# Optimization experiments

Measured on AMD Instinct MI355X. Metric: run time of the kernel, lower is better.

Reference implementation:

```python
import jax, jax.numpy as jnp
import numpy as np

NUM_CLASS = 31
B = 4096
F_IN = 2048
F_BOT = 256


def setup_inputs() -> dict:
    key = jax.random.key(0)
    ks = jax.random.split(key, 6)
    return {
        "source": jax.random.normal(ks[0], (B, F_IN), dtype=jnp.float32),
        "target": jax.random.normal(ks[1], (B, F_IN), dtype=jnp.float32),
        "W_b": jax.random.normal(ks[2], (F_IN, F_BOT), dtype=jnp.float32) * (1.0 / np.sqrt(F_IN)),
        "b_b": jnp.zeros((F_BOT,), dtype=jnp.float32),
        "W_c": jax.random.normal(ks[3], (F_BOT, NUM_CLASS), dtype=jnp.float32) * (1.0 / np.sqrt(F_BOT)),
        "b_c": jnp.zeros((NUM_CLASS,), dtype=jnp.float32),
        "source_label": jax.random.randint(ks[4], (B,), 0, NUM_CLASS, dtype=jnp.int64),
    }


def _conf_margin(logits, labels):
    # get_confidence_output_margin: softmax confidence margin vs best wrong class
    conf = jax.nn.softmax(logits, axis=-1)
    mask = jax.nn.one_hot(labels, NUM_CLASS, dtype=conf.dtype)
    targets_conf = jnp.sum(conf * mask, axis=1)
    max_excl_conf = jnp.max(conf * (1.0 - mask), axis=1)
    return targets_conf - max_excl_conf


def _pairwise_sqdist(s, t):
    # ||x_p - x_q||^2 computed as a single GEMM + broadcast (replaces python double loop)
    s2 = jnp.sum(s * s, axis=1)  # [Bs]
    t2 = jnp.sum(t * t, axis=1)  # [Bt]
    d2 = s2[:, None] + t2[None, :] - 2.0 * (s @ t.T)
    return jnp.maximum(d2, 0.0)


def reference(source, target, W_b, b_b, W_c, b_c, source_label):
    # bottleneck: Linear + ReLU (shared weights for both domains)
    src = jax.nn.relu(source @ W_b + b_b)  # [B, 256]
    tar = jax.nn.relu(target @ W_b + b_b)  # [B, 256]

    src_clf = src @ W_c + b_c  # [B, 31]
    tar_clf = tar @ W_c + b_c  # [B, 31]

    # cross entropy on source
    logp = jax.nn.log_softmax(src_clf, axis=-1)
    clf_loss = -jnp.mean(jnp.take_along_axis(logp, source_label[:, None], axis=1))

    src_margin = _conf_margin(src_clf, source_label)
    tar_margin = _conf_margin(tar_clf, jnp.argmax(tar_clf, axis=1))

    # no_grad diagnostics: MMD + Gaussian kernel means (amplitude=1, sigma in {1,5})
    delta = jnp.mean(src, axis=0) - jnp.mean(tar, axis=0)
    curr_mmd = jax.lax.stop_gradient(delta @ delta)
    d2 = _pairwise_sqdist(src, tar)  # [B, B]
    curr_gk1 = jax.lax.stop_gradient(jnp.mean(jnp.exp(-0.5 * d2)))
    curr_gk5 = jax.lax.stop_gradient(jnp.mean(jnp.exp(-d2 / 50.0)))

    return jnp.concatenate([
        jnp.stack([clf_loss, curr_mmd, curr_gk1, curr_gk5]),
        src_margin,
        tar_margin,
    ])  # [4 + 2B]
```

## Files before the change

kernel.cpp:

```cpp
#include <hip/hip_runtime.h>
#include <stdint.h>

#define DI __device__ __forceinline__

typedef float f32x4 __attribute__((ext_vector_type(4)));
typedef short bf16x8 __attribute__((ext_vector_type(8)));

DI uint16_t f2bf(float f) {
    union { float f; uint32_t u; } v; v.f = f;
    uint32_t r = v.u + 0x7FFF + ((v.u >> 16) & 1);
    return (uint16_t)(r >> 16);
}
DI float bf2f(uint16_t h) {
    union { uint32_t u; float f; } v; v.u = ((uint32_t)h) << 16;
    return v.f;
}
DI void gl_lds16(const void* g, void* l) {
    __builtin_amdgcn_global_load_lds(
        (__attribute__((address_space(1))) void*)(uintptr_t)g,
        (__attribute__((address_space(3))) void*)(uintptr_t)l,
        16, 0, 0);
}

__global__ void k_init(const float* __restrict__ Wc, uint16_t* __restrict__ WcT,
                       float* __restrict__ accs) {
    int tid = threadIdx.x;
    if (tid < 4) accs[tid] = 0.f;
    for (int idx = tid; idx < 32 * 256; idx += 256) {
        int n = idx >> 8, k = idx & 255;
        WcT[idx] = (n < 31) ? f2bf(Wc[k * 31 + n]) : (uint16_t)0;
    }
}

__global__ void k_transpose_wb(const float* __restrict__ Wb, uint16_t* __restrict__ WbT) {
    __shared__ float t[32][33];
    int kb = blockIdx.x, nb = blockIdx.y;
    int tx = threadIdx.x & 31, ty0 = (threadIdx.x >> 5) * 4;
    for (int i = 0; i < 4; ++i)
        t[ty0 + i][tx] = Wb[(kb * 32 + ty0 + i) * 256 + nb * 32 + tx];
    __syncthreads();
    for (int i = 0; i < 4; ++i)
        WbT[(nb * 32 + ty0 + i) * 2048 + kb * 32 + tx] = f2bf(t[tx][ty0 + i]);
}

__launch_bounds__(256)
__global__ void k_bottleneck(const float* __restrict__ src, const float* __restrict__ tgt,
                             const uint16_t* __restrict__ WbT, const float* __restrict__ bb,
                             uint16_t* __restrict__ Y) {
    __shared__ __align__(16) uint8_t lds[40960];
    int tid = threadIdx.x;
    int lane = tid & 63, w = tid >> 6;
    int bm = blockIdx.x >> 1, bn = blockIdx.x & 1;
    int m0 = bm * 32;
    const float* X = (m0 < 4096) ? (src + (size_t)m0 * 2048)
                                 : (tgt + (size_t)(m0 - 4096) * 2048);
    int ar = tid >> 3, akb = (tid >> 2) & 1, ap = tid & 3;
    int ac = ap ^ (ar & 3) ^ ((ar >> 2) & 3);
    const float* Ag = X + ar * 2048 + akb * 32 + ac * 8;
    const int AwOff = akb * 2048 + ar * 64 + ap * 16;
    int cc = (lane >> 4) ^ (lane & 3) ^ ((lane >> 2) & 3);
    const uint16_t* Bg0; const uint16_t* Bg1; const uint16_t* Bg2; const uint16_t* Bg3;
    {
        int p = lane & 3;
        int i0 = w * 4;
        #define BGADDR(ii) ({ int s_ = i0 + (ii); int kb_ = s_ >> 3; \
            int r_ = (s_ & 7) * 16 + (lane >> 2); \
            int c_ = p ^ (r_ & 3) ^ ((r_ >> 2) & 3); \
            WbT + (size_t)(bn * 128 + r_) * 2048 + kb_ * 32 + c_ * 8; })
        Bg0 = BGADDR(0); Bg1 = BGADDR(1); Bg2 = BGADDR(2); Bg3 = BGADDR(3);
        #undef BGADDR
    }
    const int lbB = 8192 + w * 4096;

    f32x4 acc[2][2] = {};
    float4 rE0, rE1, rO0, rO1;

    #define STAGE_B(par, k0) do { \
        gl_lds16(Bg0 + (k0), lds + lbB + (par) * 16384 + 0);    \
        gl_lds16(Bg1 + (k0), lds + lbB + (par) * 16384 + 1024); \
        gl_lds16(Bg2 + (k0), lds + lbB + (par) * 16384 + 2048); \
        gl_lds16(Bg3 + (k0), lds + lbB + (par) * 16384 + 3072); \
    } while (0)

    #define WRITE_A(par, r0v, r1v) do { \
        uint4 u_; \
        u_.x = (uint32_t)f2bf((r0v).x) | ((uint32_t)f2bf((r0v).y) << 16); \
        u_.y = (uint32_t)f2bf((r0v).z) | ((uint32_t)f2bf((r0v).w) << 16); \
        u_.z = (uint32_t)f2bf((r1v).x) | ((uint32_t)f2bf((r1v).y) << 16); \
        u_.w = (uint32_t)f2bf((r1v).z) | ((uint32_t)f2bf((r1v).w) << 16); \
        *(uint4*)(lds + (par) * 4096 + AwOff) = u_; \
    } while (0)

    #define COMPUTE(par) do { \
        _Pragma("unroll") \
        for (int kb = 0; kb < 2; ++kb) { \
            bf16x8 a_[2], b_[2]; \
            _Pragma("unroll") \
            for (int mi = 0; mi < 2; ++mi) \
                a_[mi] = *(const bf16x8*)(lds + (par) * 4096 + kb * 2048 + \
                                          (mi * 16 + (lane & 15)) * 64 + cc * 16); \
            _Pragma("unroll") \
            for (int nf = 0; nf < 2; ++nf) \
                b_[nf] = *(const bf16x8*)(lds + 8192 + (par) * 16384 + kb * 8192 + \
                                          (w * 32 + nf * 16 + (lane & 15)) * 64 + cc * 16); \
            _Pragma("unroll") \
            for (int mi = 0; mi < 2; ++mi) \
                _Pragma("unroll") \
                for (int nf = 0; nf < 2; ++nf) \
                    acc[mi][nf] = __builtin_amdgcn_mfma_f32_16x16x32_bf16( \
                        a_[mi], b_[nf], acc[mi][nf], 0, 0, 0); \
        } \
    } while (0)

    #define FENCE() asm volatile("" ::: "memory")

    STAGE_B(0, 0);
    FENCE();
    rE0 = *(const float4*)(Ag);
    rE1 = *(const float4*)(Ag + 4);
    FENCE();
    rO0 = *(const float4*)(Ag + 64);
    rO1 = *(const float4*)(Ag + 68);
    asm volatile("s_waitcnt vmcnt(2)" ::: "memory");
    WRITE_A(0, rE0, rE1);
    asm volatile("s_waitcnt lgkmcnt(0)" ::: "memory");
    __builtin_amdgcn_s_barrier();

    for (int tt = 0; tt < 15; ++tt) {
        {
            int t = 2 * tt;
            STAGE_B(1, (t + 1) * 64);
            FENCE();
            rE0 = *(const float4*)(Ag + (t + 2) * 64);
            rE1 = *(const float4*)(Ag + (t + 2) * 64 + 4);
            FENCE();
            COMPUTE(0);
            asm volatile("s_waitcnt vmcnt(6)" ::: "memory");
            WRITE_A(1, rO0, rO1);
            asm volatile("s_waitcnt vmcnt(2) lgkmcnt(0)" ::: "memory");
            __builtin_amdgcn_s_barrier();
        }
        {
            int t = 2 * tt + 1;
            STAGE_B(0, (t + 1) * 64);
            FENCE();
            rO0 = *(const float4*)(Ag + (t + 2) * 64);
            rO1 = *(const float4*)(Ag + (t + 2) * 64 + 4);
            FENCE();
            COMPUTE(1);
            asm volatile("s_waitcnt vmcnt(6)" ::: "memory");
            WRITE_A(0, rE0, rE1);
            asm volatile("s_waitcnt vmcnt(2) lgkmcnt(0)" ::: "memory");
            __builtin_amdgcn_s_barrier();
        }
    }
    STAGE_B(1, 31 * 64);
    FENCE();
    COMPUTE(0);
    asm volatile("s_waitcnt vmcnt(4)" ::: "memory");
    WRITE_A(1, rO0, rO1);
    asm volatile("s_waitcnt vmcnt(0) lgkmcnt(0)" ::: "memory");
    __builtin_amdgcn_s_barrier();
    COMPUTE(1);

    #undef STAGE_B
    #undef WRITE_A
    #undef COMPUTE
    #undef FENCE

    for (int mi = 0; mi < 2; ++mi)
        for (int nf = 0; nf < 2; ++nf) {
            int col = bn * 128 + w * 32 + nf * 16 + (lane & 15);
            float bias = bb[col];
            for (int j = 0; j < 4; ++j) {
                int row = m0 + mi * 16 + (lane >> 4) * 4 + j;
                float v = acc[mi][nf][j] + bias;
                v = fmaxf(v, 0.f);
                Y[(size_t)row * 256 + col] = f2bf(v);
            }
        }
}

__launch_bounds__(256)
__global__ void k_stats(const uint16_t* __restrict__ Y, float* __restrict__ s2t2,
                        float* __restrict__ colsum_part) {
    __shared__ float cs[4][256];
    int tid = threadIdx.x, lane = tid & 63, w = tid >> 6;
    int r0 = blockIdx.x * 32 + w * 8;
    float c0 = 0.f, c1 = 0.f, c2 = 0.f, c3 = 0.f;
    for (int i = 0; i < 8; ++i) {
        int row = r0 + i;
        ushort4 v = *(const ushort4*)(Y + (size_t)row * 256 + lane * 4);
        float a = bf2f(v.x), b = bf2f(v.y), c = bf2f(v.z), d = bf2f(v.w);
        c0 += a; c1 += b; c2 += c; c3 += d;
        float s = a * a + b * b + c * c + d * d;
        for (int m = 1; m < 64; m <<= 1) s += __shfl_xor(s, m);
        if (lane == 0) s2t2[row] = s;
    }
    cs[w][lane * 4 + 0] = c0;
    cs[w][lane * 4 + 1] = c1;
    cs[w][lane * 4 + 2] = c2;
    cs[w][lane * 4 + 3] = c3;
    __syncthreads();
    colsum_part[blockIdx.x * 256 + tid] =
        cs[0][tid] + cs[1][tid] + cs[2][tid] + cs[3][tid];
}

__launch_bounds__(256)
__global__ void k_classifier(const uint16_t* __restrict__ Y, const uint16_t* __restrict__ WcT,
                             const float* __restrict__ bc, const int* __restrict__ labels,
                             float* __restrict__ out_margin, float* __restrict__ ce_acc) {
    __shared__ __align__(16) uint8_t lds[49152];
    int tid = threadIdx.x, lane = tid & 63, w = tid >> 6;
    int m0 = blockIdx.x * 64;
    int cc = (lane >> 4) ^ (lane & 3) ^ ((lane >> 2) & 3);
    for (int s = w; s < 48; s += 4) {
        int r, p, c;
        if (s < 32) {
            int kb = s >> 2, r0 = (s & 3) * 16;
            r = r0 + (lane >> 2); p = lane & 3;
            c = p ^ (r & 3) ^ ((r >> 2) & 3);
            gl_lds16(Y + (size_t)(m0 + r) * 256 + kb * 32 + c * 8, lds + s * 1024);
        } else {
            int s2 = s - 32;
            int kb = s2 >> 1, r0 = (s2 & 1) * 16;
            r = r0 + (lane >> 2); p = lane & 3;
            c = p ^ (r & 3) ^ ((r >> 2) & 3);
            gl_lds16(WcT + r * 256 + kb * 32 + c * 8, lds + 32768 + s2 * 1024);
        }
    }
    __syncthreads();
    f32x4 acc[2] = {};
    for (int kb = 0; kb < 8; ++kb) {
        int r = w * 16 + (lane & 15);
        bf16x8 a = *(const bf16x8*)(lds + kb * 4096 + r * 64 + cc * 16);
        for (int nf = 0; nf < 2; ++nf) {
            int rn = nf * 16 + (lane & 15);
            bf16x8 b = *(const bf16x8*)(lds + 32768 + kb * 2048 + rn * 64 + cc * 16);
            acc[nf] = __builtin_amdgcn_mfma_f32_16x16x32_bf16(a, b, acc[nf], 0, 0, 0);
        }
    }
    int c0 = lane & 15, c1 = 16 + c0;
    float bc0 = bc[c0];
    float bc1 = (c1 < 31) ? bc[c1] : 0.f;
    bool is_src = (m0 < 4096);
    float ce_local = 0.f;
    for (int j = 0; j < 4; ++j) {
        int row = m0 + w * 16 + (lane >> 4) * 4 + j;
        float v0 = acc[0][j] + bc0;
        float v1 = (c1 < 31) ? (acc[1][j] + bc1) : -1e30f;
        float mx = fmaxf(v0, v1);
        for (int m = 1; m < 16; m <<= 1) mx = fmaxf(mx, __shfl_xor(mx, m, 16));
        float e0 = __expf(v0 - mx);
        float e1 = (c1 < 31) ? __expf(v1 - mx) : 0.f;
        float ssum = e0 + e1;
        for (int m = 1; m < 16; m <<= 1) ssum += __shfl_xor(ssum, m, 16);
        float inv = 1.f / ssum;
        float conf0 = e0 * inv, conf1 = e1 * inv;
        int lab;
        if (is_src) {
            lab = labels[row];
        } else {
            float bv; int bi;
            if (v0 >= v1) { bv = v0; bi = c0; } else { bv = v1; bi = c1; }
            for (int m = 1; m < 16; m <<= 1) {
                float ov = __shfl_xor(bv, m, 16);
                int oi = __shfl_xor(bi, m, 16);
                if (ov > bv || (ov == bv && oi < bi)) { bv = ov; bi = oi; }
            }
            lab = bi;
        }
        float tc = (c0 == lab ? conf0 : 0.f) + (c1 == lab ? conf1 : 0.f);
        for (int m = 1; m < 16; m <<= 1) tc += __shfl_xor(tc, m, 16);
        float ex = fmaxf(c0 == lab ? -1.f : conf0,
                         (c1 == lab || c1 >= 31) ? -1.f : conf1);
        for (int m = 1; m < 16; m <<= 1) ex = fmaxf(ex, __shfl_xor(ex, m, 16));
        if (c0 == 0) out_margin[row] = tc - ex;
        if (is_src) {
            float vl = (c0 == lab) ? v0 : ((c1 == lab) ? v1 : -1e30f);
            for (int m = 1; m < 16; m <<= 1) vl = fmaxf(vl, __shfl_xor(vl, m, 16));
            if (c0 == 0) ce_local += -(vl - mx - __logf(ssum));
        }
    }
    if (is_src) {
        ce_local += __shfl_xor(ce_local, 16);
        ce_local += __shfl_xor(ce_local, 32);
        if (lane == 0) atomicAdd(ce_acc, ce_local);
    }
}

__launch_bounds__(256)
__global__ void k_pairwise(const uint16_t* __restrict__ Y, const float* __restrict__ s2t2,
                           float* __restrict__ gk_part) {
    __shared__ __align__(16) uint8_t lds[65536];
    int tid = threadIdx.x, lane = tid & 63, w = tid >> 6;
    int m0 = blockIdx.x * 128, n0 = blockIdx.y * 128;
    int cc = (lane >> 4) ^ (lane & 3) ^ ((lane >> 2) & 3);
    int wm = (w & 1) * 64, wn = (w >> 1) * 64;
    f32x4 acc[4][4] = {};
    for (int h = 0; h < 2; ++h) {
        if (h) __syncthreads();
        int k0 = h * 128;
        for (int i = 0; i < 8; ++i) {
            int s = w * 8 + i;
            int kb = s >> 3, r0 = (s & 7) * 16;
            int r = r0 + (lane >> 2), p = lane & 3;
            int c = p ^ (r & 3) ^ ((r >> 2) & 3);
            gl_lds16(Y + (size_t)(m0 + r) * 256 + k0 + kb * 32 + c * 8, lds + s * 1024);
            gl_lds16(Y + (size_t)(4096 + n0 + r) * 256 + k0 + kb * 32 + c * 8,
                     lds + 32768 + s * 1024);
        }
        __syncthreads();
        for (int kb = 0; kb < 4; ++kb) {
            bf16x8 a[4], b[4];
            for (int mi = 0; mi < 4; ++mi) {
                int r = wm + mi * 16 + (lane & 15);
                a[mi] = *(const bf16x8*)(lds + kb * 8192 + r * 64 + cc * 16);
            }
            for (int nf = 0; nf < 4; ++nf) {
                int rn = wn + nf * 16 + (lane & 15);
                b[nf] = *(const bf16x8*)(lds + 32768 + kb * 8192 + rn * 64 + cc * 16);
            }
            for (int mi = 0; mi < 4; ++mi)
                for (int nf = 0; nf < 4; ++nf)
                    acc[mi][nf] = __builtin_amdgcn_mfma_f32_16x16x32_bf16(
                        a[mi], b[nf], acc[mi][nf], 0, 0, 0);
        }
    }
    float t2v[4];
    for (int nf = 0; nf < 4; ++nf)
        t2v[nf] = s2t2[4096 + n0 + wn + nf * 16 + (lane & 15)];
    float g1 = 0.f, g5 = 0.f;
    for (int mi = 0; mi < 4; ++mi) {
        int rbase = m0 + wm + mi * 16 + (lane >> 4) * 4;
        float s2v[4];
        for (int j = 0; j < 4; ++j) s2v[j] = s2t2[rbase + j];
        for (int nf = 0; nf < 4; ++nf)
            for (int j = 0; j < 4; ++j) {
                float d2 = s2v[j] + t2v[nf] - 2.f * acc[mi][nf][j];
                d2 = fmaxf(d2, 0.f);
                g1 += __expf(-0.5f * d2);
                g5 += __expf(-0.02f * d2);
            }
    }
    for (int m = 1; m < 64; m <<= 1) { g1 += __shfl_xor(g1, m); g5 += __shfl_xor(g5, m); }
    __syncthreads();
    float* red = (float*)lds;
    if (lane == 0) { red[w * 2] = g1; red[w * 2 + 1] = g5; }
    __syncthreads();
    if (tid == 0) {
        int bid = blockIdx.y * 32 + blockIdx.x;
        gk_part[bid * 2]     = red[0] + red[2] + red[4] + red[6];
        gk_part[bid * 2 + 1] = red[1] + red[3] + red[5] + red[7];
    }
}

__global__ void k_finalize(const float* __restrict__ colsum_part,
                           const float* __restrict__ gk_part,
                           const float* __restrict__ accs, float* __restrict__ d_out) {
    __shared__ float red[12];
    int tid = threadIdx.x, lane = tid & 63, w = tid >> 6;
    float cs = 0.f, ct = 0.f;
    for (int b = 0; b < 128; ++b)   cs += colsum_part[b * 256 + tid];
    for (int b = 128; b < 256; ++b) ct += colsum_part[b * 256 + tid];
    float delta = (cs - ct) * (1.f / 4096.f);
    float sq = delta * delta;
    float g1 = 0.f, g5 = 0.f;
    for (int i = 0; i < 4; ++i) {
        int p = tid * 4 + i;
        g1 += gk_part[p * 2];
        g5 += gk_part[p * 2 + 1];
    }
    for (int m = 1; m < 64; m <<= 1) {
        sq += __shfl_xor(sq, m);
        g1 += __shfl_xor(g1, m);
        g5 += __shfl_xor(g5, m);
    }
    if (lane == 0) { red[w * 3] = sq; red[w * 3 + 1] = g1; red[w * 3 + 2] = g5; }
    __syncthreads();
    if (tid == 0) {
        d_out[0] = accs[0] * (1.f / 4096.f);
        d_out[1] = red[0] + red[3] + red[6] + red[9];
        d_out[2] = (red[1] + red[4] + red[7] + red[10]) * 5.9604644775390625e-08f;
        d_out[3] = (red[2] + red[5] + red[8] + red[11]) * 5.9604644775390625e-08f;
    }
}

extern "C" void kernel_launch(void* const* d_in, const int* in_sizes, int n_in,
                              void* d_out, int out_size, void* d_ws, size_t ws_size,
                              hipStream_t stream) {
    const float* source = (const float*)d_in[0];
    const float* target = (const float*)d_in[1];
    const float* Wb     = (const float*)d_in[2];
    const float* bb     = (const float*)d_in[3];
    const float* Wc     = (const float*)d_in[4];
    const float* bc     = (const float*)d_in[5];
    const int*   labels = (const int*)d_in[6];
    float* out = (float*)d_out;
    uint8_t* ws = (uint8_t*)d_ws;

    uint16_t* Y    = (uint16_t*)(ws);
    uint16_t* WbT  = (uint16_t*)(ws + 4194304);
    uint16_t* WcT  = (uint16_t*)(ws + 5242880);
    float*    s2t2 = (float*)(ws + 5259264);
    float*    accs = (float*)(ws + 5292032);
    float*    colsum_part = (float*)(ws + 4194304);
    float*    gk_part     = (float*)(ws + 4194304 + 262144);

    k_init<<<1, 256, 0, stream>>>(Wc, WcT, accs);
    k_transpose_wb<<<dim3(64, 8), 256, 0, stream>>>(Wb, WbT);
    k_bottleneck<<<512, 256, 0, stream>>>(source, target, WbT, bb, Y);
    k_stats<<<256, 256, 0, stream>>>(Y, s2t2, colsum_part);
    k_classifier<<<128, 256, 0, stream>>>(Y, WcT, bc, labels, out + 4, accs);
    k_pairwise<<<dim3(32, 32), 256, 0, stream>>>(Y, s2t2, gk_part);
    k_finalize<<<1, 256, 0, stream>>>(colsum_part, gk_part, accs, out);
}
```

Before: 174.6 us.

## Narrow bottleneck GEMM N-tile to 64 and triple-buffer W_b staging

The bottleneck GEMM tile shrinks from 32x128 to 32x64 per block, which doubles the grid to 1024 blocks and cuts LDS per block to 32 KB so more blocks fit on each CU. The B operand staging moves from double to triple buffering with a two-stage-ahead prefetch and uniform vmcnt(4) waits, unrolled by six to rotate buffers. The cost is that each A row block (the fp32 activations) is now loaded and converted four times instead of twice, which raises global traffic on the dominant 64 MB input read.

```diff
diff --git a/kernel.cpp b/kernel.cpp
--- a/kernel.cpp
+++ b/kernel.cpp
@@ -47,10 +47,10 @@
 __global__ void k_bottleneck(const float* __restrict__ src, const float* __restrict__ tgt,
                              const uint16_t* __restrict__ WbT, const float* __restrict__ bb,
                              uint16_t* __restrict__ Y) {
-    __shared__ __align__(16) uint8_t lds[40960];
+    __shared__ __align__(16) uint8_t lds[32768];
     int tid = threadIdx.x;
     int lane = tid & 63, w = tid >> 6;
-    int bm = blockIdx.x >> 1, bn = blockIdx.x & 1;
+    int bm = blockIdx.x >> 2, bn = blockIdx.x & 3;
     int m0 = bm * 32;
     const float* X = (m0 < 4096) ? (src + (size_t)m0 * 2048)
                                  : (tgt + (size_t)(m0 - 4096) * 2048);
@@ -59,27 +59,27 @@
     const float* Ag = X + ar * 2048 + akb * 32 + ac * 8;
     const int AwOff = akb * 2048 + ar * 64 + ap * 16;
     int cc = (lane >> 4) ^ (lane & 3) ^ ((lane >> 2) & 3);
-    const uint16_t* Bg0; const uint16_t* Bg1; const uint16_t* Bg2; const uint16_t* Bg3;
+    const uint16_t* Bg0; const uint16_t* Bg1;
+    int lb0, lb1;
     {
         int p = lane & 3;
-        int i0 = w * 4;
-        #define BGADDR(ii) ({ int s_ = i0 + (ii); int kb_ = s_ >> 3; \
-            int r_ = (s_ & 7) * 16 + (lane >> 2); \
+        #define BGADDR(ii) ({ int s_ = w * 2 + (ii); int kb_ = s_ >> 2; \
+            int r_ = (s_ & 3) * 16 + (lane >> 2); \
             int c_ = p ^ (r_ & 3) ^ ((r_ >> 2) & 3); \
-            WbT + (size_t)(bn * 128 + r_) * 2048 + kb_ * 32 + c_ * 8; })
-        Bg0 = BGADDR(0); Bg1 = BGADDR(1); Bg2 = BGADDR(2); Bg3 = BGADDR(3);
+            WbT + (size_t)(bn * 64 + r_) * 2048 + kb_ * 32 + c_ * 8; })
+        Bg0 = BGADDR(0); Bg1 = BGADDR(1);
         #undef BGADDR
-    }
-    const int lbB = 8192 + w * 4096;
-
-    f32x4 acc[2][2] = {};
+        lb0 = (w * 2 + 0) * 1024;
+        lb1 = (w * 2 + 1) * 1024;
+    }
+    int rnOff = (w * 16 + (lane & 15)) * 64 + cc * 16;
+
+    f32x4 acc[2] = {};
     float4 rE0, rE1, rO0, rO1;
 
-    #define STAGE_B(par, k0) do { \
-        gl_lds16(Bg0 + (k0), lds + lbB + (par) * 16384 + 0);    \
-        gl_lds16(Bg1 + (k0), lds + lbB + (par) * 16384 + 1024); \
-        gl_lds16(Bg2 + (k0), lds + lbB + (par) * 16384 + 2048); \
-        gl_lds16(Bg3 + (k0), lds + lbB + (par) * 16384 + 3072); \
+    #define STAGE_B(buf, k0) do { \
+        gl_lds16(Bg0 + (k0), lds + 8192 + (buf) * 8192 + lb0); \
+        gl_lds16(Bg1 + (k0), lds + 8192 + (buf) * 8192 + lb1); \
     } while (0)
 
     #define WRITE_A(par, r0v, r1v) do { \
@@ -91,94 +91,89 @@
         *(uint4*)(lds + (par) * 4096 + AwOff) = u_; \
     } while (0)
 
-    #define COMPUTE(par) do { \
+    #define COMPUTE(buf, par) do { \
         _Pragma("unroll") \
         for (int kb = 0; kb < 2; ++kb) { \
-            bf16x8 a_[2], b_[2]; \
+            bf16x8 a_[2], b_; \
             _Pragma("unroll") \
             for (int mi = 0; mi < 2; ++mi) \
                 a_[mi] = *(const bf16x8*)(lds + (par) * 4096 + kb * 2048 + \
                                           (mi * 16 + (lane & 15)) * 64 + cc * 16); \
-            _Pragma("unroll") \
-            for (int nf = 0; nf < 2; ++nf) \
-                b_[nf] = *(const bf16x8*)(lds + 8192 + (par) * 16384 + kb * 8192 + \
-                                          (w * 32 + nf * 16 + (lane & 15)) * 64 + cc * 16); \
+            b_ = *(const bf16x8*)(lds + 8192 + (buf) * 8192 + kb * 4096 + rnOff); \
             _Pragma("unroll") \
             for (int mi = 0; mi < 2; ++mi) \
-                _Pragma("unroll") \
-                for (int nf = 0; nf < 2; ++nf) \
-                    acc[mi][nf] = __builtin_amdgcn_mfma_f32_16x16x32_bf16( \
-                        a_[mi], b_[nf], acc[mi][nf], 0, 0, 0); \
+                acc[mi] = __builtin_amdgcn_mfma_f32_16x16x32_bf16( \
+                    a_[mi], b_, acc[mi], 0, 0, 0); \
         } \
     } while (0)
 
     #define FENCE() asm volatile("" ::: "memory")
+    #define WAIT4() asm volatile("s_waitcnt vmcnt(4)" ::: "memory")
+    #define WAIT0() asm volatile("s_waitcnt vmcnt(0)" ::: "memory")
+    #define LGKM0_BAR() do { asm volatile("s_waitcnt lgkmcnt(0)" ::: "memory"); \
+                             __builtin_amdgcn_s_barrier(); } while (0)
 
     STAGE_B(0, 0);
     FENCE();
     rE0 = *(const float4*)(Ag);
     rE1 = *(const float4*)(Ag + 4);
     FENCE();
+    STAGE_B(1, 64);
+    FENCE();
     rO0 = *(const float4*)(Ag + 64);
     rO1 = *(const float4*)(Ag + 68);
-    asm volatile("s_waitcnt vmcnt(2)" ::: "memory");
+    WAIT4();
     WRITE_A(0, rE0, rE1);
-    asm volatile("s_waitcnt lgkmcnt(0)" ::: "memory");
-    __builtin_amdgcn_s_barrier();
-
-    for (int tt = 0; tt < 15; ++tt) {
-        {
-            int t = 2 * tt;
-            STAGE_B(1, (t + 1) * 64);
-            FENCE();
-            rE0 = *(const float4*)(Ag + (t + 2) * 64);
-            rE1 = *(const float4*)(Ag + (t + 2) * 64 + 4);
-            FENCE();
-            COMPUTE(0);
-            asm volatile("s_waitcnt vmcnt(6)" ::: "memory");
-            WRITE_A(1, rO0, rO1);
-            asm volatile("s_waitcnt vmcnt(2) lgkmcnt(0)" ::: "memory");
-            __builtin_amdgcn_s_barrier();
-        }
-        {
-            int t = 2 * tt + 1;
-            STAGE_B(0, (t + 1) * 64);
-            FENCE();
-            rO0 = *(const float4*)(Ag + (t + 2) * 64);
-            rO1 = *(const float4*)(Ag + (t + 2) * 64 + 4);
-            FENCE();
-            COMPUTE(1);
-            asm volatile("s_waitcnt vmcnt(6)" ::: "memory");
-            WRITE_A(0, rE0, rE1);
-            asm volatile("s_waitcnt vmcnt(2) lgkmcnt(0)" ::: "memory");
-            __builtin_amdgcn_s_barrier();
-        }
-    }
-    STAGE_B(1, 31 * 64);
-    FENCE();
-    COMPUTE(0);
-    asm volatile("s_waitcnt vmcnt(4)" ::: "memory");
+    LGKM0_BAR();
+
+    #define ITER(tc, BUF, NBUF, RL0, RL1, RW0, RW1, WPAR) do { \
+        STAGE_B(NBUF, ((tc) + 2) * 64); \
+        FENCE(); \
+        RL0 = *(const float4*)(Ag + ((tc) + 2) * 64); \
+        RL1 = *(const float4*)(Ag + ((tc) + 2) * 64 + 4); \
+        FENCE(); \
+        COMPUTE(BUF, (tc) & 1); \
+        WAIT4();  \
+        WRITE_A(WPAR, RW0, RW1); \
+        LGKM0_BAR(); \
+    } while (0)
+
+    for (int t6 = 0; t6 < 5; ++t6) {
+        int tb = t6 * 6;
+        ITER(tb + 0, 0, 2, rE0, rE1, rO0, rO1, 1);
+        ITER(tb + 1, 1, 0, rO0, rO1, rE0, rE1, 0);
+        ITER(tb + 2, 2, 1, rE0, rE1, rO0, rO1, 1);
+        ITER(tb + 3, 0, 2, rO0, rO1, rE0, rE1, 0);
+        ITER(tb + 4, 1, 0, rE0, rE1, rO0, rO1, 1);
+        ITER(tb + 5, 2, 1, rO0, rO1, rE0, rE1, 0);
+    }
+    COMPUTE(0, 0);
+    WAIT0();
     WRITE_A(1, rO0, rO1);
-    asm volatile("s_waitcnt vmcnt(0) lgkmcnt(0)" ::: "memory");
-    __builtin_amdgcn_s_barrier();
-    COMPUTE(1);
-
+    LGKM0_BAR();
+    COMPUTE(1, 1);
+
+    #undef ITER
     #undef STAGE_B
     #undef WRITE_A
     #undef COMPUTE
     #undef FENCE
-
-    for (int mi = 0; mi < 2; ++mi)
-        for (int nf = 0; nf < 2; ++nf) {
-            int col = bn * 128 + w * 32 + nf * 16 + (lane & 15);
-            float bias = bb[col];
+    #undef WAIT4
+    #undef WAIT0
+    #undef LGKM0_BAR
+
+    {
+        int col = bn * 64 + w * 16 + (lane & 15);
+        float bias = bb[col];
+        for (int mi = 0; mi < 2; ++mi) {
             for (int j = 0; j < 4; ++j) {
                 int row = m0 + mi * 16 + (lane >> 4) * 4 + j;
-                float v = acc[mi][nf][j] + bias;
+                float v = acc[mi][j] + bias;
                 v = fmaxf(v, 0.f);
                 Y[(size_t)row * 256 + col] = f2bf(v);
             }
         }
+    }
 }
 
 __launch_bounds__(256)
@@ -409,7 +404,7 @@
 
     k_init<<<1, 256, 0, stream>>>(Wc, WcT, accs);
     k_transpose_wb<<<dim3(64, 8), 256, 0, stream>>>(Wb, WbT);
-    k_bottleneck<<<512, 256, 0, stream>>>(source, target, WbT, bb, Y);
+    k_bottleneck<<<1024, 256, 0, stream>>>(source, target, WbT, bb, Y);
     k_stats<<<256, 256, 0, stream>>>(Y, s2t2, colsum_part);
     k_classifier<<<128, 256, 0, stream>>>(Y, WcT, bc, labels, out + 4, accs);
     k_pairwise<<<dim3(32, 32), 256, 0, stream>>>(Y, s2t2, gk_part);
```

After: 184.2 us. 1.05x slower.
